# Kernel tuning notes

Hardware: AMD Instinct MI355X
Metric: run time of the kernel (lower is better)

Reference implementation:

```python
import jax, jax.numpy as jnp
import numpy as np

NUM_RAYS = 8192
NUM_INTERS = 32
POS_DIMS = 10 * 6 + 3   # 63
DIR_DIMS = 4 * 6 + 3    # 27
UNITS = 256
APP_DIMS = 48


def _linear_params(key, fan_in, fan_out):
    kw, kb = jax.random.split(key)
    bound = 1.0 / np.sqrt(fan_in)
    W = jax.random.uniform(kw, (fan_in, fan_out), minval=-bound, maxval=bound, dtype=jnp.float32)
    b = jax.random.uniform(kb, (fan_out,), minval=-bound, maxval=bound, dtype=jnp.float32)
    return W, b


def setup_inputs() -> dict:
    key = jax.random.key(0)
    ks = jax.random.split(key, 14)
    N = NUM_RAYS * NUM_INTERS
    inp = {
        "pos_encodings": jax.random.normal(ks[0], (N, POS_DIMS), dtype=jnp.float32),
        "dir_encodings": jax.random.normal(ks[1], (N, DIR_DIMS), dtype=jnp.float32),
        "app_encodings": jax.random.normal(ks[2], (1, APP_DIMS), dtype=jnp.float32),
        "gemo_encodings": jax.random.normal(ks[3], (N, UNITS), dtype=jnp.float32),
        "color_encodings": jax.random.normal(ks[4], (N, UNITS), dtype=jnp.float32),
        "mask": jax.random.uniform(ks[5], (N,), dtype=jnp.float32),
        "num_inters": NUM_INTERS,
    }
    inp["W0"], inp["b0"] = _linear_params(ks[6], POS_DIMS, UNITS)
    inp["W1"], inp["b1"] = _linear_params(ks[7], UNITS, UNITS)
    inp["W2"], inp["b2"] = _linear_params(ks[8], UNITS * 2, UNITS)
    inp["Ws"], inp["bs"] = _linear_params(ks[9], UNITS, 1)
    inp["W3"], inp["b3"] = _linear_params(ks[10], UNITS * 2, UNITS)
    inp["W4"], inp["b4"] = _linear_params(ks[11], DIR_DIMS + UNITS + APP_DIMS, UNITS)
    inp["Wr"], inp["br"] = _linear_params(ks[12], UNITS, 3)
    return inp


def reference(pos_encodings, dir_encodings, app_encodings, gemo_encodings,
              color_encodings, mask, num_inters,
              W0, b0, W1, b1, W2, b2, Ws, bs, W3, b3, W4, b4, Wr, br):
    N = NUM_RAYS * num_inters
    app = jnp.tile(app_encodings, (N, 1))                       # [N, app_dims]
    d0 = jax.nn.relu(pos_encodings @ W0 + b0)                   # [N, U]
    d1 = jax.nn.relu(d0 @ W1 + b1)                              # [N, U]
    d2 = jax.nn.relu(jnp.concatenate([d1, gemo_encodings], -1) @ W2 + b2)
    sigmas = jax.nn.softplus(d2 @ Ws + bs)[:, 0] * mask         # [N]
    d3 = jax.nn.relu(jnp.concatenate([d1, color_encodings], -1) @ W3 + b3)
    d4 = jax.nn.relu(jnp.concatenate([d3, dir_encodings, app], -1) @ W4 + b4)
    rgbs = jax.nn.sigmoid(d4 @ Wr + br)                         # [N, 3]
    return (sigmas.reshape(NUM_RAYS, num_inters),
            rgbs.reshape(NUM_RAYS, num_inters, 3))
```

## Files before the change

kernel.cpp:

```cpp
#include <hip/hip_runtime.h>


typedef __bf16 bf16x8 __attribute__((ext_vector_type(8)));
typedef float  f32x4  __attribute__((ext_vector_type(4)));
typedef short  short8 __attribute__((ext_vector_type(8)));
typedef unsigned int uint4v __attribute__((ext_vector_type(4)));

#define NROWS (8192 * 32)
#define MT 64
#define RS 260

#define P0B   0
#define P1B   16384
#define P2B   81920
#define P3B   212992
#define P4AB  344064
#define P4BB  409600
#define PTOT  417792

#define ACT_ELEMS (64 * RS)
#define SMEM_BYTES (ACT_ELEMS * 2 + 4 * 8192 + 3072)

__device__ __forceinline__ unsigned short f2bf(float f) {
  unsigned u = __builtin_bit_cast(unsigned, f);
  u += 0x7fffu + ((u >> 16) & 1u);
  return (unsigned short)(u >> 16);
}
__device__ __forceinline__ unsigned cvt_pk(float lo, float hi) {
  unsigned r;
  asm("v_cvt_pk_bf16_f32 %0, %1, %2" : "=v"(r) : "v"(lo), "v"(hi));
  return r;
}
__device__ __forceinline__ bf16x8 cvt8(f32x4 x, f32x4 y) {
  uint4v u;
  u[0] = cvt_pk(x[0], x[1]); u[1] = cvt_pk(x[2], x[3]);
  u[2] = cvt_pk(y[0], y[1]); u[3] = cvt_pk(y[2], y[3]);
  return __builtin_bit_cast(bf16x8, u);
}
__device__ __forceinline__ bf16x8 as_bf(short8 s) {
  return __builtin_bit_cast(bf16x8, s);
}

#define SB __builtin_amdgcn_sched_barrier(0)

#define GLDS16(gsrc, ldst)                                                     \
  __builtin_amdgcn_global_load_lds(                                            \
      (const __attribute__((address_space(1))) unsigned int*)(gsrc),           \
      (__attribute__((address_space(3))) unsigned int*)(ldst), 16, 0, 0)

__global__ void prep_pack(const float* __restrict__ W0, const float* __restrict__ W1,
                          const float* __restrict__ W2, const float* __restrict__ W3,
                          const float* __restrict__ W4, const float* __restrict__ Wr,
                          const float* __restrict__ app, const float* __restrict__ b4,
                          unsigned short* __restrict__ pack, float* __restrict__ b4p,
                          float* __restrict__ wrT)
{
  int gid = blockIdx.x * 256 + threadIdx.x;
  if (gid < PTOT) {
    const float* W; int Kreal, base, krow = 0;
    if      (gid < P1B)  { W = W0; Kreal = 63;  base = P0B; }
    else if (gid < P2B)  { W = W1; Kreal = 256; base = P1B; }
    else if (gid < P3B)  { W = W2; Kreal = 512; base = P2B; }
    else if (gid < P4AB) { W = W3; Kreal = 512; base = P3B; }
    else if (gid < P4BB) { W = W4; Kreal = 256; base = P4AB; }
    else                 { W = W4; Kreal = 27;  base = P4BB; krow = 256; }
    int local = gid - base;
    int j   = local & 7;
    int l16 = (local >> 3) & 15;
    int seg = (local >> 7) & 3;
    int ct  = (local >> 9) & 3;
    int wv  = (local >> 11) & 3;
    int kt  = local >> 13;
    int o = wv * 64 + ct * 16 + l16;
    int k = kt * 32 + seg * 8 + j;
    float v = (k < Kreal) ? W[(long)(k + krow) * 256 + o] : 0.f;
    pack[gid] = f2bf(v);
  } else if (gid < PTOT + 256) {
    int o = gid - PTOT;
    float a = b4[o];
    for (int i = 0; i < 48; ++i) a += app[i] * W4[(long)(283 + i) * 256 + o];
    b4p[o] = a;
  } else if (gid < PTOT + 256 + 768) {
    int idx = gid - (PTOT + 256);
    int c = idx >> 8, ch = idx & 255;
    wrT[c * 256 + ch] = Wr[ch * 3 + c];
  }
}

__global__ __launch_bounds__(256, 2)
void nerf_fused(const float* __restrict__ pos, const float* __restrict__ dirs,
                const float* __restrict__ gemo, const float* __restrict__ color,
                const float* __restrict__ mask,
                const unsigned short* __restrict__ wp,
                const float* __restrict__ b0, const float* __restrict__ b1,
                const float* __restrict__ b2, const float* __restrict__ bsv,
                const float* __restrict__ b3, const float* __restrict__ b4p,
                const float* __restrict__ brv,
                const float* __restrict__ Wsf, const float* __restrict__ wrT,
                float* __restrict__ osig, float* __restrict__ orgb)
{
  extern __shared__ unsigned short smem[];
  unsigned short* act  = smem;
  unsigned short* ring = smem + ACT_ELEMS;
  float* scr = (float*)(smem + ACT_ELEMS + 4 * 4096);

  const int tid  = (int)threadIdx.x;
  const int w    = tid >> 6;
  const int lane = tid & 63;
  const int l16  = lane & 15;
  const int seg  = lane >> 4;
  const int chb  = w * 64;
  const long R0  = (long)blockIdx.x * MT;
  const int rot  = (int)(blockIdx.x & 7);

  f32x4 acc[4][4];

  auto stageB = [&](const float* __restrict__ P, int slot, int c) {
#pragma unroll
    for (int m = 0; m < 2; ++m) {
      int u = m * 256 + w * 64 + lane;
      int row = u >> 3;
      int part = (u & 7) ^ (row & 7);
      const float* src = P + (R0 + row) * 256 + c * 32 + part * 4;
      unsigned short* dst = ring + slot * 4096 + (m * 256 + w * 64) * 8;
      GLDS16(src, dst);
    }
  };
  auto ldB_ring = [&](int slot, int rt, int p) -> f32x4 {
    int row = rt * 16 + l16;
    return *(const f32x4*)(ring + slot * 4096 + (row * 8 + (p ^ (row & 7))) * 8);
  };
  auto ldAd = [&](int baseElems, int kt, int ct) -> bf16x8 {
    return *(const bf16x8*)(wp + baseElems + kt * 8192 + w * 2048 +
                            ((ct * 4 + seg) * 16 + l16) * 8);
  };
  auto ldB_act = [&](int rt, int kt) -> bf16x8 {
    int row = rt * 16 + l16;
    return *(const bf16x8*)(act + row * RS + kt * 32 + seg * 8);
  };
  auto ldB_gen = [&](const float* __restrict__ p, int stride, int Kreal,
                     int rt, int ktl) -> bf16x8 {
    long row = R0 + rt * 16 + l16;
    const float* q = p + row * stride;
    int k0 = ktl * 32 + seg * 8;
    short8 s;
#pragma unroll
    for (int j = 0; j < 8; ++j) {
      float v = (k0 + j < Kreal) ? __builtin_nontemporal_load(q + k0 + j) : 0.0f;
      s[j] = (short)f2bf(v);
    }
    return as_bf(s);
  };
  auto initAcc = [&](const float* __restrict__ b) {
#pragma unroll
    for (int ct = 0; ct < 4; ++ct) {
      float4 bv = *(const float4*)(b + chb + ct * 16 + seg * 4);
      f32x4 t; t[0] = bv.x; t[1] = bv.y; t[2] = bv.z; t[3] = bv.w;
#pragma unroll
      for (int rt = 0; rt < 4; ++rt) acc[ct][rt] = t;
    }
  };
  auto storeAct = [&]() {
#pragma unroll
    for (int ct = 0; ct < 4; ++ct)
#pragma unroll
      for (int rt = 0; rt < 4; ++rt) {
        int row = rt * 16 + l16;
        int ch  = chb + ct * 16 + seg * 4;
        f32x4 v = acc[ct][rt];
        uint2 u;
        u.x = cvt_pk(fmaxf(v[0], 0.f), fmaxf(v[1], 0.f));
        u.y = cvt_pk(fmaxf(v[2], 0.f), fmaxf(v[3], 0.f));
        *(uint2*)(act + row * RS + ch) = u;
      }
  };

#define MFMA16(AEXPR, BFRAGS)                                                  \
  _Pragma("unroll") for (int ct = 0; ct < 4; ++ct) {                           \
    bf16x8 Af_ = (AEXPR);                                                      \
    _Pragma("unroll") for (int rt = 0; rt < 4; ++rt)                           \
      acc[ct][rt] = __builtin_amdgcn_mfma_f32_16x16x32_bf16(                   \
          Af_, BFRAGS[rt], acc[ct][rt], 0, 0, 0);                              \
  }

#define LHALF(ABASE)                                                           \
  _Pragma("unroll") for (int i = 0; i < 8; ++i) {                              \
    int kt = (i + rot) & 7;                                                    \
    bf16x8 Bf_[4];                                                             \
    _Pragma("unroll") for (int rt = 0; rt < 4; ++rt) Bf_[rt] = ldB_act(rt, kt); \
    MFMA16(ldAd(ABASE, kt, ct), Bf_);                                          \
  }

#define GREG(i, NFENCE)                                                        \
  {                                                                            \
    asm volatile("s_waitcnt vmcnt(" #NFENCE ")" ::: "memory");                 \
    SB;                                                                        \
    __builtin_amdgcn_s_barrier();                                              \
    if ((i) + 2 < 8) {                                                         \
      _Pragma("unroll") for (int ct = 0; ct < 4; ++ct)                         \
        AfG[((i) + 2) % 3][ct] = ldAd(GABASE, 8 + (((i) + 2 + rot) & 7), ct);  \
    }                                                                          \
    if ((i) + 3 < 8) stageB(GP, ((i) + 3) & 3, ((i) + 3 + rot) & 7);           \
    SB;                                                                        \
    bf16x8 Bf_[4];                                                             \
    _Pragma("unroll") for (int rt = 0; rt < 4; ++rt) {                         \
      f32x4 lo = ldB_ring((i) & 3, rt, 2 * seg);                               \
      f32x4 hi = ldB_ring((i) & 3, rt, 2 * seg + 1);                           \
      Bf_[rt] = cvt8(lo, hi);                                                  \
    }                                                                          \
    _Pragma("unroll") for (int ct = 0; ct < 4; ++ct) {                         \
      _Pragma("unroll") for (int rt = 0; rt < 4; ++rt)                         \
        acc[ct][rt] = __builtin_amdgcn_mfma_f32_16x16x32_bf16(                 \
            AfG[(i) % 3][ct], Bf_[rt], acc[ct][rt], 0, 0, 0);                  \
    }                                                                          \
  }

#define GHALF(ABASE, P)                                                        \
  {                                                                            \
    const int GABASE = (ABASE); const float* __restrict__ GP = (P);            \
    bf16x8 AfG[3][4];                                                          \
    SB;                                                                        \
    _Pragma("unroll") for (int ct = 0; ct < 4; ++ct) {                         \
      AfG[0][ct] = ldAd(GABASE, 8 + ((0 + rot) & 7), ct);                      \
      AfG[1][ct] = ldAd(GABASE, 8 + ((1 + rot) & 7), ct);                      \
    }                                                                          \
    SB;                                                                        \
    GREG(0, 12) GREG(1, 12) GREG(2, 12) GREG(3, 12)                            \
    GREG(4, 12) GREG(5, 12) GREG(6, 10) GREG(7, 4)                             \
  }

  initAcc(b0);
#pragma unroll
  for (int kt = 0; kt < 2; ++kt) {
    bf16x8 Bf_[4];
#pragma unroll
    for (int rt = 0; rt < 4; ++rt) Bf_[rt] = ldB_gen(pos, 63, 63, rt, kt);
    MFMA16(ldAd(P0B, kt, ct), Bf_);
  }
  storeAct();
  __syncthreads();

  initAcc(b1);
  LHALF(P1B);
  __syncthreads();
  storeAct();
  __syncthreads();

  stageB(gemo, 0, rot);
  stageB(gemo, 1, (1 + rot) & 7);
  stageB(gemo, 2, (2 + rot) & 7);
  initAcc(b2);
  LHALF(P2B);
  GHALF(P2B, gemo);

  {
    float p[4];
#pragma unroll
    for (int rt = 0; rt < 4; ++rt) {
      float s = 0.f;
#pragma unroll
      for (int ct = 0; ct < 4; ++ct) {
        float4 w4 = *(const float4*)(Wsf + chb + ct * 16 + seg * 4);
        f32x4 a = acc[ct][rt];
        s += fmaxf(a[0], 0.f) * w4.x + fmaxf(a[1], 0.f) * w4.y +
             fmaxf(a[2], 0.f) * w4.z + fmaxf(a[3], 0.f) * w4.w;
      }
      s += __shfl_xor(s, 16);
      s += __shfl_xor(s, 32);
      p[rt] = s;
    }
    if (seg == 0) {
#pragma unroll
      for (int rt = 0; rt < 4; ++rt) scr[w * 64 + rt * 16 + l16] = p[rt];
    }
  }
  __syncthreads();
  if (tid < 64) {
    float s = scr[tid] + scr[64 + tid] + scr[128 + tid] + scr[192 + tid] + bsv[0];
    float sp = fmaxf(s, 0.f) + log1pf(expf(-fabsf(s)));
    float m = __builtin_nontemporal_load(mask + R0 + tid);
    __builtin_nontemporal_store(sp * m, osig + R0 + tid);
  }

  stageB(color, 0, rot);
  stageB(color, 1, (1 + rot) & 7);
  stageB(color, 2, (2 + rot) & 7);
  initAcc(b3);
  LHALF(P3B);
  GHALF(P3B, color);
  __syncthreads();
  storeAct();
  __syncthreads();

  initAcc(b4p);
  LHALF(P4AB);
  {
    bf16x8 Bf_[4];
#pragma unroll
    for (int rt = 0; rt < 4; ++rt) Bf_[rt] = ldB_gen(dirs, 27, 27, rt, 0);
    MFMA16(ldAd(P4BB, 0, ct), Bf_);
  }

  {
#pragma unroll
    for (int ct = 0; ct < 4; ++ct)
#pragma unroll
      for (int rt = 0; rt < 4; ++rt) {
        f32x4 a = acc[ct][rt];
        a[0] = fmaxf(a[0], 0.f); a[1] = fmaxf(a[1], 0.f);
        a[2] = fmaxf(a[2], 0.f); a[3] = fmaxf(a[3], 0.f);
        acc[ct][rt] = a;
      }
#pragma unroll
    for (int c = 0; c < 3; ++c) {
      float p[4];
#pragma unroll
      for (int rt = 0; rt < 4; ++rt) {
        float s = 0.f;
#pragma unroll
        for (int ct = 0; ct < 4; ++ct) {
          float4 w4 = *(const float4*)(wrT + c * 256 + chb + ct * 16 + seg * 4);
          f32x4 a = acc[ct][rt];
          s += a[0] * w4.x + a[1] * w4.y + a[2] * w4.z + a[3] * w4.w;
        }
        s += __shfl_xor(s, 16);
        s += __shfl_xor(s, 32);
        p[rt] = s;
      }
      if (seg == 0) {
#pragma unroll
        for (int rt = 0; rt < 4; ++rt)
          scr[c * 256 + w * 64 + rt * 16 + l16] = p[rt];
      }
    }
  }
  __syncthreads();
  if (tid < 64) {
#pragma unroll
    for (int c = 0; c < 3; ++c) {
      float s = scr[c * 256 + tid] + scr[c * 256 + 64 + tid] +
                scr[c * 256 + 128 + tid] + scr[c * 256 + 192 + tid] + brv[c];
      float r = 1.f / (1.f + expf(-s));
      __builtin_nontemporal_store(r, orgb + (R0 + tid) * 3 + c);
    }
  }
#undef MFMA16
#undef LHALF
#undef GREG
#undef GHALF
}

extern "C" void kernel_launch(void* const* d_in, const int* in_sizes, int n_in,
                              void* d_out, int out_size, void* d_ws, size_t ws_size,
                              hipStream_t stream) {
  const float* pos   = (const float*)d_in[0];
  const float* dirs  = (const float*)d_in[1];
  const float* app   = (const float*)d_in[2];
  const float* gemo  = (const float*)d_in[3];
  const float* color = (const float*)d_in[4];
  const float* mask  = (const float*)d_in[5];
  const float* W0 = (const float*)d_in[7];   const float* b0 = (const float*)d_in[8];
  const float* W1 = (const float*)d_in[9];   const float* b1 = (const float*)d_in[10];
  const float* W2 = (const float*)d_in[11];  const float* b2 = (const float*)d_in[12];
  const float* Ws = (const float*)d_in[13];  const float* bs = (const float*)d_in[14];
  const float* W3 = (const float*)d_in[15];  const float* b3 = (const float*)d_in[16];
  const float* W4 = (const float*)d_in[17];  const float* b4 = (const float*)d_in[18];
  const float* Wr = (const float*)d_in[19];  const float* br = (const float*)d_in[20];

  unsigned short* pack = (unsigned short*)d_ws;
  float* b4p = (float*)((char*)d_ws + (size_t)PTOT * 2);
  float* wrT = b4p + 256;

  float* osig = (float*)d_out;
  float* orgb = osig + NROWS;

  prep_pack<<<dim3((PTOT + 256 + 768 + 255) / 256), dim3(256), 0, stream>>>(
      W0, W1, W2, W3, W4, Wr, app, b4, pack, b4p, wrT);

  hipFuncSetAttribute((const void*)nerf_fused,
                      hipFuncAttributeMaxDynamicSharedMemorySize, SMEM_BYTES);

  nerf_fused<<<dim3(NROWS / MT), dim3(256), SMEM_BYTES, stream>>>(
      pos, dirs, gemo, color, mask, pack,
      b0, b1, b2, bs, b3, b4p, br, Ws, wrT, osig, orgb);
}
```

Measured before the change: 453.7 us.

## Interleave activation and global-input halves per K-step with software-pipelined A fragments

Measured after the change: 465.5 us. 2.6% more time.

```diff
diff --git a/kernel.cpp b/kernel.cpp
--- a/kernel.cpp
+++ b/kernel.cpp
@@ -42,6 +42,8 @@
 }
 
 #define SB __builtin_amdgcn_sched_barrier(0)
+#define LBAR do { asm volatile("s_waitcnt lgkmcnt(0)" ::: "memory");           \
+                  __builtin_amdgcn_s_barrier(); SB; } while (0)
 
 #define GLDS16(gsrc, ldst)                                                     \
   __builtin_amdgcn_global_load_lds(                                            \
@@ -175,58 +177,93 @@
       }
   };
 
-#define MFMA16(AEXPR, BFRAGS)                                                  \
+#define MFMA16(AFRAG, BFRAGS)                                                  \
   _Pragma("unroll") for (int ct = 0; ct < 4; ++ct) {                           \
-    bf16x8 Af_ = (AEXPR);                                                      \
     _Pragma("unroll") for (int rt = 0; rt < 4; ++rt)                           \
       acc[ct][rt] = __builtin_amdgcn_mfma_f32_16x16x32_bf16(                   \
-          Af_, BFRAGS[rt], acc[ct][rt], 0, 0, 0);                              \
-  }
-
-#define LHALF(ABASE)                                                           \
-  _Pragma("unroll") for (int i = 0; i < 8; ++i) {                              \
-    int kt = (i + rot) & 7;                                                    \
-    bf16x8 Bf_[4];                                                             \
-    _Pragma("unroll") for (int rt = 0; rt < 4; ++rt) Bf_[rt] = ldB_act(rt, kt); \
-    MFMA16(ldAd(ABASE, kt, ct), Bf_);                                          \
-  }
-
-#define GREG(i, NFENCE)                                                        \
+          AFRAG[ct], BFRAGS[rt], acc[ct][rt], 0, 0, 0);                        \
+  }
+
+#define ISTEP(i, NF)                                                           \
   {                                                                            \
-    asm volatile("s_waitcnt vmcnt(" #NFENCE ")" ::: "memory");                 \
+    asm volatile("s_waitcnt vmcnt(" #NF ")" ::: "memory"); SB;                 \
+    __builtin_amdgcn_s_barrier(); SB;                                          \
+    if ((i) + 2 < 8) {                                                         \
+      _Pragma("unroll") for (int ct = 0; ct < 4; ++ct) {                       \
+        AfG[((i) + 2) % 3][ct] = ldAd(IBASE, 8 + (((i) + 2 + rot) & 7), ct);   \
+        AfL[((i) + 2) % 3][ct] = ldAd(IBASE, (((i) + 2 + rot) & 7), ct);       \
+      }                                                                        \
+    }                                                                          \
+    if ((i) + 3 < 8) stageB(IP, ((i) + 3) & 3, ((i) + 3 + rot) & 7);           \
     SB;                                                                        \
-    __builtin_amdgcn_s_barrier();                                              \
+    __builtin_amdgcn_s_setprio(1);                                             \
+    {                                                                          \
+      bf16x8 Bf_[4];                                                           \
+      _Pragma("unroll") for (int rt = 0; rt < 4; ++rt) {                       \
+        f32x4 lo = ldB_ring((i) & 3, rt, 2 * seg);                             \
+        f32x4 hi = ldB_ring((i) & 3, rt, 2 * seg + 1);                         \
+        Bf_[rt] = cvt8(lo, hi);                                                \
+      }                                                                        \
+      MFMA16(AfG[(i) % 3], Bf_);                                               \
+    }                                                                          \
+    {                                                                          \
+      bf16x8 Bf_[4];                                                           \
+      _Pragma("unroll") for (int rt = 0; rt < 4; ++rt)                         \
+        Bf_[rt] = ldB_act(rt, ((i) + rot) & 7);                                \
+      MFMA16(AfL[(i) % 3], Bf_);                                               \
+    }                                                                          \
+    __builtin_amdgcn_s_setprio(0);                                             \
+  }
+
+#define ILAYER(ABASE, P)                                                       \
+  {                                                                            \
+    const int IBASE = (ABASE); const float* __restrict__ IP = (P);             \
+    bf16x8 AfG[3][4], AfL[3][4];                                               \
+    SB; stageB(IP, 0, rot & 7); SB;                                            \
+    _Pragma("unroll") for (int ct = 0; ct < 4; ++ct) {                         \
+      AfG[0][ct] = ldAd(IBASE, 8 + (rot & 7), ct);                             \
+      AfL[0][ct] = ldAd(IBASE, (rot & 7), ct);                                 \
+    }                                                                          \
+    stageB(IP, 1, (1 + rot) & 7); SB;                                          \
+    _Pragma("unroll") for (int ct = 0; ct < 4; ++ct) {                         \
+      AfG[1][ct] = ldAd(IBASE, 8 + ((1 + rot) & 7), ct);                       \
+      AfL[1][ct] = ldAd(IBASE, ((1 + rot) & 7), ct);                           \
+    }                                                                          \
+    stageB(IP, 2, (2 + rot) & 7); SB;                                          \
+    ISTEP(0, 20) ISTEP(1, 20) ISTEP(2, 20) ISTEP(3, 20)                        \
+    ISTEP(4, 20) ISTEP(5, 20) ISTEP(6, 18) ISTEP(7, 8)                         \
+  }
+
+#define LSTEP(i)                                                               \
+  {                                                                            \
+    SB;                                                                        \
     if ((i) + 2 < 8) {                                                         \
       _Pragma("unroll") for (int ct = 0; ct < 4; ++ct)                         \
-        AfG[((i) + 2) % 3][ct] = ldAd(GABASE, 8 + (((i) + 2 + rot) & 7), ct);  \
-    }                                                                          \
-    if ((i) + 3 < 8) stageB(GP, ((i) + 3) & 3, ((i) + 3 + rot) & 7);           \
+        AfL[((i) + 2) % 3][ct] = ldAd(LBASE, (((i) + 2 + rot) & 7), ct);       \
+    }                                                                          \
     SB;                                                                        \
-    bf16x8 Bf_[4];                                                             \
-    _Pragma("unroll") for (int rt = 0; rt < 4; ++rt) {                         \
-      f32x4 lo = ldB_ring((i) & 3, rt, 2 * seg);                               \
-      f32x4 hi = ldB_ring((i) & 3, rt, 2 * seg + 1);                           \
-      Bf_[rt] = cvt8(lo, hi);                                                  \
-    }                                                                          \
-    _Pragma("unroll") for (int ct = 0; ct < 4; ++ct) {                         \
+    __builtin_amdgcn_s_setprio(1);                                             \
+    {                                                                          \
+      bf16x8 Bf_[4];                                                           \
       _Pragma("unroll") for (int rt = 0; rt < 4; ++rt)                         \
-        acc[ct][rt] = __builtin_amdgcn_mfma_f32_16x16x32_bf16(                 \
-            AfG[(i) % 3][ct], Bf_[rt], acc[ct][rt], 0, 0, 0);                  \
-    }                                                                          \
-  }
-
-#define GHALF(ABASE, P)                                                        \
+        Bf_[rt] = ldB_act(rt, ((i) + rot) & 7);                                \
+      MFMA16(AfL[(i) % 3], Bf_);                                               \
+    }                                                                          \
+    __builtin_amdgcn_s_setprio(0);                                             \
+  }
+
+#define LLAYER(ABASE)                                                          \
   {                                                                            \
-    const int GABASE = (ABASE); const float* __restrict__ GP = (P);            \
-    bf16x8 AfG[3][4];                                                          \
+    const int LBASE = (ABASE);                                                 \
+    bf16x8 AfL[3][4];                                                          \
     SB;                                                                        \
     _Pragma("unroll") for (int ct = 0; ct < 4; ++ct) {                         \
-      AfG[0][ct] = ldAd(GABASE, 8 + ((0 + rot) & 7), ct);                      \
-      AfG[1][ct] = ldAd(GABASE, 8 + ((1 + rot) & 7), ct);                      \
+      AfL[0][ct] = ldAd(LBASE, (rot & 7), ct);                                 \
+      AfL[1][ct] = ldAd(LBASE, ((1 + rot) & 7), ct);                           \
     }                                                                          \
     SB;                                                                        \
-    GREG(0, 12) GREG(1, 12) GREG(2, 12) GREG(3, 12)                            \
-    GREG(4, 12) GREG(5, 12) GREG(6, 10) GREG(7, 4)                             \
+    LSTEP(0) LSTEP(1) LSTEP(2) LSTEP(3)                                        \
+    LSTEP(4) LSTEP(5) LSTEP(6) LSTEP(7)                                        \
   }
 
   initAcc(b0);
@@ -235,23 +272,22 @@
     bf16x8 Bf_[4];
 #pragma unroll
     for (int rt = 0; rt < 4; ++rt) Bf_[rt] = ldB_gen(pos, 63, 63, rt, kt);
-    MFMA16(ldAd(P0B, kt, ct), Bf_);
+    bf16x8 Af_[4];
+#pragma unroll
+    for (int ct = 0; ct < 4; ++ct) Af_[ct] = ldAd(P0B, kt, ct);
+    MFMA16(Af_, Bf_);
   }
   storeAct();
-  __syncthreads();
+  LBAR;
 
   initAcc(b1);
-  LHALF(P1B);
-  __syncthreads();
+  LLAYER(P1B);
+  LBAR;
   storeAct();
-  __syncthreads();
-
-  stageB(gemo, 0, rot);
-  stageB(gemo, 1, (1 + rot) & 7);
-  stageB(gemo, 2, (2 + rot) & 7);
+  LBAR;
+
   initAcc(b2);
-  LHALF(P2B);
-  GHALF(P2B, gemo);
+  ILAYER(P2B, gemo);
 
   {
     float p[4];
@@ -274,7 +310,7 @@
       for (int rt = 0; rt < 4; ++rt) scr[w * 64 + rt * 16 + l16] = p[rt];
     }
   }
-  __syncthreads();
+  LBAR;
   if (tid < 64) {
     float s = scr[tid] + scr[64 + tid] + scr[128 + tid] + scr[192 + tid] + bsv[0];
     float sp = fmaxf(s, 0.f) + log1pf(expf(-fabsf(s)));
@@ -282,23 +318,22 @@
     __builtin_nontemporal_store(sp * m, osig + R0 + tid);
   }
 
-  stageB(color, 0, rot);
-  stageB(color, 1, (1 + rot) & 7);
-  stageB(color, 2, (2 + rot) & 7);
   initAcc(b3);
-  LHALF(P3B);
-  GHALF(P3B, color);
-  __syncthreads();
+  ILAYER(P3B, color);
+  LBAR;
   storeAct();
-  __syncthreads();
+  LBAR;
 
   initAcc(b4p);
-  LHALF(P4AB);
+  LLAYER(P4AB);
   {
     bf16x8 Bf_[4];
 #pragma unroll
     for (int rt = 0; rt < 4; ++rt) Bf_[rt] = ldB_gen(dirs, 27, 27, rt, 0);
-    MFMA16(ldAd(P4BB, 0, ct), Bf_);
+    bf16x8 Af_[4];
+#pragma unroll
+    for (int ct = 0; ct < 4; ++ct) Af_[ct] = ldAd(P4BB, 0, ct);
+    MFMA16(Af_, Bf_);
   }
 
   {
@@ -334,7 +369,7 @@
       }
     }
   }
-  __syncthreads();
+  LBAR;
   if (tid < 64) {
 #pragma unroll
     for (int c = 0; c < 3; ++c) {
@@ -345,9 +380,10 @@
     }
   }
 #undef MFMA16
-#undef LHALF
-#undef GREG
-#undef GHALF
+#undef ISTEP
+#undef ILAYER
+#undef LSTEP
+#undef LLAYER
 }
 
 extern "C" void kernel_launch(void* const* d_in, const int* in_sizes, int n_in,
```

## Halve row tile to 32 rows per block and double occupancy target

Applied to the files above, without the earlier changes.

After: 532.7 us. 1.17x slower.

```diff
diff --git a/kernel.cpp b/kernel.cpp
--- a/kernel.cpp
+++ b/kernel.cpp
@@ -7,7 +7,7 @@
 typedef unsigned int uint4v __attribute__((ext_vector_type(4)));
 
 #define NROWS (8192 * 32)
-#define MT 64
+#define MT 32
 #define RS 260
 
 #define P0B   0
@@ -18,8 +18,8 @@
 #define P4BB  409600
 #define PTOT  417792
 
-#define ACT_ELEMS (64 * RS)
-#define SMEM_BYTES (ACT_ELEMS * 2 + 4 * 8192 + 3072)
+#define ACT_ELEMS (MT * RS)
+#define SMEM_BYTES (ACT_ELEMS * 2 + 4 * 4096 + 1536)
 
 __device__ __forceinline__ unsigned short f2bf(float f) {
   unsigned u = __builtin_bit_cast(unsigned, f);
@@ -87,7 +87,7 @@
   }
 }
 
-__global__ __launch_bounds__(256, 2)
+__global__ __launch_bounds__(256, 4)
 void nerf_fused(const float* __restrict__ pos, const float* __restrict__ dirs,
                 const float* __restrict__ gemo, const float* __restrict__ color,
                 const float* __restrict__ mask,
@@ -102,7 +102,7 @@
   extern __shared__ unsigned short smem[];
   unsigned short* act  = smem;
   unsigned short* ring = smem + ACT_ELEMS;
-  float* scr = (float*)(smem + ACT_ELEMS + 4 * 4096);
+  float* scr = (float*)(smem + ACT_ELEMS + 4 * 2048);
 
   const int tid  = (int)threadIdx.x;
   const int w    = tid >> 6;
@@ -113,22 +113,19 @@
   const long R0  = (long)blockIdx.x * MT;
   const int rot  = (int)(blockIdx.x & 7);
 
-  f32x4 acc[4][4];
+  f32x4 acc[4][2];
 
   auto stageB = [&](const float* __restrict__ P, int slot, int c) {
-#pragma unroll
-    for (int m = 0; m < 2; ++m) {
-      int u = m * 256 + w * 64 + lane;
-      int row = u >> 3;
-      int part = (u & 7) ^ (row & 7);
-      const float* src = P + (R0 + row) * 256 + c * 32 + part * 4;
-      unsigned short* dst = ring + slot * 4096 + (m * 256 + w * 64) * 8;
-      GLDS16(src, dst);
-    }
+    int u = tid;
+    int row = u >> 3;
+    int part = (u & 7) ^ (row & 7);
+    const float* src = P + (R0 + row) * 256 + c * 32 + part * 4;
+    unsigned short* dst = ring + slot * 2048 + u * 8;
+    GLDS16(src, dst);
   };
   auto ldB_ring = [&](int slot, int rt, int p) -> f32x4 {
     int row = rt * 16 + l16;
-    return *(const f32x4*)(ring + slot * 4096 + (row * 8 + (p ^ (row & 7))) * 8);
+    return *(const f32x4*)(ring + slot * 2048 + (row * 8 + (p ^ (row & 7))) * 8);
   };
   auto ldAd = [&](int baseElems, int kt, int ct) -> bf16x8 {
     return *(const bf16x8*)(wp + baseElems + kt * 8192 + w * 2048 +
@@ -157,14 +154,14 @@
       float4 bv = *(const float4*)(b + chb + ct * 16 + seg * 4);
       f32x4 t; t[0] = bv.x; t[1] = bv.y; t[2] = bv.z; t[3] = bv.w;
 #pragma unroll
-      for (int rt = 0; rt < 4; ++rt) acc[ct][rt] = t;
+      for (int rt = 0; rt < 2; ++rt) acc[ct][rt] = t;
     }
   };
   auto storeAct = [&]() {
 #pragma unroll
     for (int ct = 0; ct < 4; ++ct)
 #pragma unroll
-      for (int rt = 0; rt < 4; ++rt) {
+      for (int rt = 0; rt < 2; ++rt) {
         int row = rt * 16 + l16;
         int ch  = chb + ct * 16 + seg * 4;
         f32x4 v = acc[ct][rt];
@@ -175,44 +172,40 @@
       }
   };
 
-#define MFMA16(AEXPR, BFRAGS)                                                  \
+#define MFMA8(AFRAG, BFRAGS)                                                   \
   _Pragma("unroll") for (int ct = 0; ct < 4; ++ct) {                           \
-    bf16x8 Af_ = (AEXPR);                                                      \
-    _Pragma("unroll") for (int rt = 0; rt < 4; ++rt)                           \
+    _Pragma("unroll") for (int rt = 0; rt < 2; ++rt)                           \
       acc[ct][rt] = __builtin_amdgcn_mfma_f32_16x16x32_bf16(                   \
-          Af_, BFRAGS[rt], acc[ct][rt], 0, 0, 0);                              \
+          AFRAG[ct], BFRAGS[rt], acc[ct][rt], 0, 0, 0);                        \
   }
 
 #define LHALF(ABASE)                                                           \
   _Pragma("unroll") for (int i = 0; i < 8; ++i) {                              \
     int kt = (i + rot) & 7;                                                    \
-    bf16x8 Bf_[4];                                                             \
-    _Pragma("unroll") for (int rt = 0; rt < 4; ++rt) Bf_[rt] = ldB_act(rt, kt); \
-    MFMA16(ldAd(ABASE, kt, ct), Bf_);                                          \
-  }
-
-#define GREG(i, NFENCE)                                                        \
+    bf16x8 Bf_[2];                                                             \
+    _Pragma("unroll") for (int rt = 0; rt < 2; ++rt) Bf_[rt] = ldB_act(rt, kt); \
+    bf16x8 Af_[4];                                                             \
+    _Pragma("unroll") for (int ct = 0; ct < 4; ++ct) Af_[ct] = ldAd(ABASE, kt, ct); \
+    MFMA8(Af_, Bf_);                                                           \
+  }
+
+#define GREG(i, NF)                                                            \
   {                                                                            \
-    asm volatile("s_waitcnt vmcnt(" #NFENCE ")" ::: "memory");                 \
-    SB;                                                                        \
-    __builtin_amdgcn_s_barrier();                                              \
+    asm volatile("s_waitcnt vmcnt(" #NF ")" ::: "memory"); SB;                 \
+    __builtin_amdgcn_s_barrier(); SB;                                          \
     if ((i) + 2 < 8) {                                                         \
       _Pragma("unroll") for (int ct = 0; ct < 4; ++ct)                         \
         AfG[((i) + 2) % 3][ct] = ldAd(GABASE, 8 + (((i) + 2 + rot) & 7), ct);  \
     }                                                                          \
     if ((i) + 3 < 8) stageB(GP, ((i) + 3) & 3, ((i) + 3 + rot) & 7);           \
     SB;                                                                        \
-    bf16x8 Bf_[4];                                                             \
-    _Pragma("unroll") for (int rt = 0; rt < 4; ++rt) {                         \
+    bf16x8 Bf_[2];                                                             \
+    _Pragma("unroll") for (int rt = 0; rt < 2; ++rt) {                         \
       f32x4 lo = ldB_ring((i) & 3, rt, 2 * seg);                               \
       f32x4 hi = ldB_ring((i) & 3, rt, 2 * seg + 1);                           \
       Bf_[rt] = cvt8(lo, hi);                                                  \
     }                                                                          \
-    _Pragma("unroll") for (int ct = 0; ct < 4; ++ct) {                         \
-      _Pragma("unroll") for (int rt = 0; rt < 4; ++rt)                         \
-        acc[ct][rt] = __builtin_amdgcn_mfma_f32_16x16x32_bf16(                 \
-            AfG[(i) % 3][ct], Bf_[rt], acc[ct][rt], 0, 0, 0);                  \
-    }                                                                          \
+    MFMA8(AfG[(i) % 3], Bf_);                                                  \
   }
 
 #define GHALF(ABASE, P)                                                        \
@@ -225,17 +218,20 @@
       AfG[1][ct] = ldAd(GABASE, 8 + ((1 + rot) & 7), ct);                      \
     }                                                                          \
     SB;                                                                        \
-    GREG(0, 12) GREG(1, 12) GREG(2, 12) GREG(3, 12)                            \
-    GREG(4, 12) GREG(5, 12) GREG(6, 10) GREG(7, 4)                             \
+    GREG(0, 10) GREG(1, 10) GREG(2, 10) GREG(3, 10)                            \
+    GREG(4, 10) GREG(5, 10) GREG(6, 9)  GREG(7, 4)                             \
   }
 
   initAcc(b0);
 #pragma unroll
   for (int kt = 0; kt < 2; ++kt) {
-    bf16x8 Bf_[4];
-#pragma unroll
-    for (int rt = 0; rt < 4; ++rt) Bf_[rt] = ldB_gen(pos, 63, 63, rt, kt);
-    MFMA16(ldAd(P0B, kt, ct), Bf_);
+    bf16x8 Bf_[2];
+#pragma unroll
+    for (int rt = 0; rt < 2; ++rt) Bf_[rt] = ldB_gen(pos, 63, 63, rt, kt);
+    bf16x8 Af_[4];
+#pragma unroll
+    for (int ct = 0; ct < 4; ++ct) Af_[ct] = ldAd(P0B, kt, ct);
+    MFMA8(Af_, Bf_);
   }
   storeAct();
   __syncthreads();
@@ -254,9 +250,9 @@
   GHALF(P2B, gemo);
 
   {
-    float p[4];
-#pragma unroll
-    for (int rt = 0; rt < 4; ++rt) {
+    float p[2];
+#pragma unroll
+    for (int rt = 0; rt < 2; ++rt) {
       float s = 0.f;
 #pragma unroll
       for (int ct = 0; ct < 4; ++ct) {
@@ -271,12 +267,12 @@
     }
     if (seg == 0) {
 #pragma unroll
-      for (int rt = 0; rt < 4; ++rt) scr[w * 64 + rt * 16 + l16] = p[rt];
-    }
-  }
-  __syncthreads();
-  if (tid < 64) {
-    float s = scr[tid] + scr[64 + tid] + scr[128 + tid] + scr[192 + tid] + bsv[0];
+      for (int rt = 0; rt < 2; ++rt) scr[w * 32 + rt * 16 + l16] = p[rt];
+    }
+  }
+  __syncthreads();
+  if (tid < 32) {
+    float s = scr[tid] + scr[32 + tid] + scr[64 + tid] + scr[96 + tid] + bsv[0];
     float sp = fmaxf(s, 0.f) + log1pf(expf(-fabsf(s)));
     float m = __builtin_nontemporal_load(mask + R0 + tid);
     __builtin_nontemporal_store(sp * m, osig + R0 + tid);
@@ -295,17 +291,20 @@
   initAcc(b4p);
   LHALF(P4AB);
   {
-    bf16x8 Bf_[4];
-#pragma unroll
-    for (int rt = 0; rt < 4; ++rt) Bf_[rt] = ldB_gen(dirs, 27, 27, rt, 0);
-    MFMA16(ldAd(P4BB, 0, ct), Bf_);
+    bf16x8 Bf_[2];
+#pragma unroll
+    for (int rt = 0; rt < 2; ++rt) Bf_[rt] = ldB_gen(dirs, 27, 27, rt, 0);
+    bf16x8 Af_[4];
+#pragma unroll
+    for (int ct = 0; ct < 4; ++ct) Af_[ct] = ldAd(P4BB, 0, ct);
+    MFMA8(Af_, Bf_);
   }
 
   {
 #pragma unroll
     for (int ct = 0; ct < 4; ++ct)
 #pragma unroll
-      for (int rt = 0; rt < 4; ++rt) {
+      for (int rt = 0; rt < 2; ++rt) {
         f32x4 a = acc[ct][rt];
         a[0] = fmaxf(a[0], 0.f); a[1] = fmaxf(a[1], 0.f);
         a[2] = fmaxf(a[2], 0.f); a[3] = fmaxf(a[3], 0.f);
@@ -313,9 +312,9 @@
       }
 #pragma unroll
     for (int c = 0; c < 3; ++c) {
-      float p[4];
-#pragma unroll
-      for (int rt = 0; rt < 4; ++rt) {
+      float p[2];
+#pragma unroll
+      for (int rt = 0; rt < 2; ++rt) {
         float s = 0.f;
 #pragma unroll
         for (int ct = 0; ct < 4; ++ct) {
@@ -329,22 +328,22 @@
       }
       if (seg == 0) {
 #pragma unroll
-        for (int rt = 0; rt < 4; ++rt)
-          scr[c * 256 + w * 64 + rt * 16 + l16] = p[rt];
-      }
-    }
-  }
-  __syncthreads();
-  if (tid < 64) {
+        for (int rt = 0; rt < 2; ++rt)
+          scr[c * 128 + w * 32 + rt * 16 + l16] = p[rt];
+      }
+    }
+  }
+  __syncthreads();
+  if (tid < 32) {
 #pragma unroll
     for (int c = 0; c < 3; ++c) {
-      float s = scr[c * 256 + tid] + scr[c * 256 + 64 + tid] +
-                scr[c * 256 + 128 + tid] + scr[c * 256 + 192 + tid] + brv[c];
+      float s = scr[c * 128 + tid] + scr[c * 128 + 32 + tid] +
+                scr[c * 128 + 64 + tid] + scr[c * 128 + 96 + tid] + brv[c];
       float r = 1.f / (1.f + expf(-s));
       __builtin_nontemporal_store(r, orgb + (R0 + tid) * 3 + c);
     }
   }
-#undef MFMA16
+#undef MFMA8
 #undef LHALF
 #undef GREG
 #undef GHALF
```

## Shrink streamed-input ring from four to two slots with shallower prefetch

Applied to the files above, without the earlier changes.

After: 472.4 us. +4.1%, slower.

```diff
diff --git a/kernel.cpp b/kernel.cpp
--- a/kernel.cpp
+++ b/kernel.cpp
@@ -18,8 +18,8 @@
 #define P4BB  409600
 #define PTOT  417792
 
-#define ACT_ELEMS (64 * RS)
-#define SMEM_BYTES (ACT_ELEMS * 2 + 4 * 8192 + 3072)
+#define ACT_ELEMS (MT * RS)
+#define SMEM_BYTES (ACT_ELEMS * 2 + 2 * 8192 + 3072)
 
 __device__ __forceinline__ unsigned short f2bf(float f) {
   unsigned u = __builtin_bit_cast(unsigned, f);
@@ -102,7 +102,7 @@
   extern __shared__ unsigned short smem[];
   unsigned short* act  = smem;
   unsigned short* ring = smem + ACT_ELEMS;
-  float* scr = (float*)(smem + ACT_ELEMS + 4 * 4096);
+  float* scr = (float*)(smem + ACT_ELEMS + 2 * 4096);
 
   const int tid  = (int)threadIdx.x;
   const int w    = tid >> 6;
@@ -175,12 +175,11 @@
       }
   };
 
-#define MFMA16(AEXPR, BFRAGS)                                                  \
+#define MFMA16(AFRAG, BFRAGS)                                                  \
   _Pragma("unroll") for (int ct = 0; ct < 4; ++ct) {                           \
-    bf16x8 Af_ = (AEXPR);                                                      \
     _Pragma("unroll") for (int rt = 0; rt < 4; ++rt)                           \
       acc[ct][rt] = __builtin_amdgcn_mfma_f32_16x16x32_bf16(                   \
-          Af_, BFRAGS[rt], acc[ct][rt], 0, 0, 0);                              \
+          AFRAG[ct], BFRAGS[rt], acc[ct][rt], 0, 0, 0);                        \
   }
 
 #define LHALF(ABASE)                                                           \
@@ -188,45 +187,40 @@
     int kt = (i + rot) & 7;                                                    \
     bf16x8 Bf_[4];                                                             \
     _Pragma("unroll") for (int rt = 0; rt < 4; ++rt) Bf_[rt] = ldB_act(rt, kt); \
-    MFMA16(ldAd(ABASE, kt, ct), Bf_);                                          \
-  }
-
-#define GREG(i, NFENCE)                                                        \
+    bf16x8 Af_[4];                                                             \
+    _Pragma("unroll") for (int ct = 0; ct < 4; ++ct) Af_[ct] = ldAd(ABASE, kt, ct); \
+    MFMA16(Af_, Bf_);                                                          \
+  }
+
+#define GREG(i, NF)                                                            \
   {                                                                            \
-    asm volatile("s_waitcnt vmcnt(" #NFENCE ")" ::: "memory");                 \
-    SB;                                                                        \
-    __builtin_amdgcn_s_barrier();                                              \
-    if ((i) + 2 < 8) {                                                         \
+    asm volatile("s_waitcnt vmcnt(" #NF ")" ::: "memory"); SB;                 \
+    __builtin_amdgcn_s_barrier(); SB;                                          \
+    if ((i) + 1 < 8) {                                                         \
+      stageB(GP, ((i) + 1) & 1, ((i) + 1 + rot) & 7);                          \
       _Pragma("unroll") for (int ct = 0; ct < 4; ++ct)                         \
-        AfG[((i) + 2) % 3][ct] = ldAd(GABASE, 8 + (((i) + 2 + rot) & 7), ct);  \
+        AfG[((i) + 1) & 1][ct] = ldAd(GABASE, 8 + (((i) + 1 + rot) & 7), ct);  \
     }                                                                          \
-    if ((i) + 3 < 8) stageB(GP, ((i) + 3) & 3, ((i) + 3 + rot) & 7);           \
     SB;                                                                        \
     bf16x8 Bf_[4];                                                             \
     _Pragma("unroll") for (int rt = 0; rt < 4; ++rt) {                         \
-      f32x4 lo = ldB_ring((i) & 3, rt, 2 * seg);                               \
-      f32x4 hi = ldB_ring((i) & 3, rt, 2 * seg + 1);                           \
+      f32x4 lo = ldB_ring((i) & 1, rt, 2 * seg);                               \
+      f32x4 hi = ldB_ring((i) & 1, rt, 2 * seg + 1);                           \
       Bf_[rt] = cvt8(lo, hi);                                                  \
     }                                                                          \
-    _Pragma("unroll") for (int ct = 0; ct < 4; ++ct) {                         \
-      _Pragma("unroll") for (int rt = 0; rt < 4; ++rt)                         \
-        acc[ct][rt] = __builtin_amdgcn_mfma_f32_16x16x32_bf16(                 \
-            AfG[(i) % 3][ct], Bf_[rt], acc[ct][rt], 0, 0, 0);                  \
-    }                                                                          \
+    MFMA16(AfG[(i) & 1], Bf_);                                                 \
   }
 
 #define GHALF(ABASE, P)                                                        \
   {                                                                            \
     const int GABASE = (ABASE); const float* __restrict__ GP = (P);            \
-    bf16x8 AfG[3][4];                                                          \
+    bf16x8 AfG[2][4];                                                          \
     SB;                                                                        \
-    _Pragma("unroll") for (int ct = 0; ct < 4; ++ct) {                         \
-      AfG[0][ct] = ldAd(GABASE, 8 + ((0 + rot) & 7), ct);                      \
-      AfG[1][ct] = ldAd(GABASE, 8 + ((1 + rot) & 7), ct);                      \
-    }                                                                          \
+    _Pragma("unroll") for (int ct = 0; ct < 4; ++ct)                           \
+      AfG[0][ct] = ldAd(GABASE, 8 + (rot & 7), ct);                            \
     SB;                                                                        \
-    GREG(0, 12) GREG(1, 12) GREG(2, 12) GREG(3, 12)                            \
-    GREG(4, 12) GREG(5, 12) GREG(6, 10) GREG(7, 4)                             \
+    GREG(0, 4) GREG(1, 4) GREG(2, 4) GREG(3, 4)                                \
+    GREG(4, 4) GREG(5, 4) GREG(6, 4) GREG(7, 0)                                \
   }
 
   initAcc(b0);
@@ -235,7 +229,10 @@
     bf16x8 Bf_[4];
 #pragma unroll
     for (int rt = 0; rt < 4; ++rt) Bf_[rt] = ldB_gen(pos, 63, 63, rt, kt);
-    MFMA16(ldAd(P0B, kt, ct), Bf_);
+    bf16x8 Af_[4];
+#pragma unroll
+    for (int ct = 0; ct < 4; ++ct) Af_[ct] = ldAd(P0B, kt, ct);
+    MFMA16(Af_, Bf_);
   }
   storeAct();
   __syncthreads();
@@ -246,9 +243,7 @@
   storeAct();
   __syncthreads();
 
-  stageB(gemo, 0, rot);
-  stageB(gemo, 1, (1 + rot) & 7);
-  stageB(gemo, 2, (2 + rot) & 7);
+  SB; stageB(gemo, 0, rot & 7); SB;
   initAcc(b2);
   LHALF(P2B);
   GHALF(P2B, gemo);
@@ -282,9 +277,7 @@
     __builtin_nontemporal_store(sp * m, osig + R0 + tid);
   }
 
-  stageB(color, 0, rot);
-  stageB(color, 1, (1 + rot) & 7);
-  stageB(color, 2, (2 + rot) & 7);
+  SB; stageB(color, 0, rot & 7); SB;
   initAcc(b3);
   LHALF(P3B);
   GHALF(P3B, color);
@@ -298,7 +291,10 @@
     bf16x8 Bf_[4];
 #pragma unroll
     for (int rt = 0; rt < 4; ++rt) Bf_[rt] = ldB_gen(dirs, 27, 27, rt, 0);
-    MFMA16(ldAd(P4BB, 0, ct), Bf_);
+    bf16x8 Af_[4];
+#pragma unroll
+    for (int ct = 0; ct < 4; ++ct) Af_[ct] = ldAd(P4BB, 0, ct);
+    MFMA16(Af_, Bf_);
   }
 
   {
```
